# Performance work log

Measured on AMD Instinct MI355X. Metric: run time of the kernel, lower is better.

The kernel has to match this reference:

```python
import jax, jax.numpy as jnp
import numpy as np

E = 100000   # number of edges
S = 64       # multiplicity of 0e (scalar) irreps
V = 32       # multiplicity of 1o (vector) irreps; also number of gates
RS3 = 1.0 / np.sqrt(3.0)   # wigner_3j constant for (1,1,0)/(0,1,1)/(1,0,1) paths
RS6 = 1.0 / np.sqrt(6.0)   # (unused here: no 1o output from 1o x 1o)

# per-path normalization: 1/sqrt(n_paths_to_slot * mul1 * mul2), e3nn-style 'uvw'
A_SS_S = (2.0 * S * S) ** -0.5
A_VV_S = (2.0 * V * V) ** -0.5 * RS3
A_SS_G = (2.0 * S * S) ** -0.5
A_VV_G = (2.0 * V * V) ** -0.5 * RS3
A_SV_V = (2.0 * S * V) ** -0.5 * RS3
A_VS_V = (2.0 * V * S) ** -0.5 * RS3


def setup_inputs() -> dict:
    key = jax.random.key(0)
    ks = jax.random.split(key, 12)
    d_in = S + 3 * V
    return {
        "fea_in1": jax.random.normal(ks[0], (E, d_in), jnp.float32),
        "fea_in2": jax.random.normal(ks[1], (E, d_in), jnp.float32),
        "fea_weight": jax.random.normal(ks[2], (E, V), jnp.float32),   # unused (kept for signature parity)
        "batch_edge": jax.random.randint(ks[3], (E,), 0, 16, jnp.int32),  # unused (norm='')
        # SeparateWeightTensorProduct ('uvw') weights, one tensor per CG path
        "w_ss_s": jax.random.normal(ks[4], (S, S, S), jnp.float32),  # 0e x 0e -> 0e (scalars)
        "w_vv_s": jax.random.normal(ks[5], (V, V, S), jnp.float32),  # 1o x 1o -> 0e (scalars)
        "w_ss_g": jax.random.normal(ks[6], (S, S, V), jnp.float32),  # 0e x 0e -> 0e (gates)
        "w_vv_g": jax.random.normal(ks[7], (V, V, V), jnp.float32),  # 1o x 1o -> 0e (gates)
        "w_sv_v": jax.random.normal(ks[8], (S, V, V), jnp.float32),  # 0e x 1o -> 1o
        "w_vs_v": jax.random.normal(ks[9], (V, S, V), jnp.float32),  # 1o x 0e -> 1o
        # equivariant o3.Linear weights (channel mixing per irrep, shared over m)
        "wl_s": jax.random.normal(ks[10], (S, S), jnp.float32),
        "wl_v": jax.random.normal(ks[11], (V, V), jnp.float32),
    }


def reference(fea_in1, fea_in2, fea_weight, batch_edge,
              w_ss_s, w_vv_s, w_ss_g, w_vv_g, w_sv_v, w_vs_v, wl_s, wl_v):
    # split flattened irreps features: [S scalars | V vectors * 3]
    s1 = fea_in1[:, :S]
    v1 = fea_in1[:, S:].reshape(-1, V, 3)
    s2 = fea_in2[:, :S]
    v2 = fea_in2[:, S:].reshape(-1, V, 3)

    # --- separate-weight tensor product (fully connected 'uvw' paths) ---
    z_s = (A_SS_S * jnp.einsum('uvw,eu,ev->ew', w_ss_s, s1, s2)
           + A_VV_S * jnp.einsum('uvw,eui,evi->ew', w_vv_s, v1, v2))   # (E,S) 0e
    z_g = (A_SS_G * jnp.einsum('uvw,eu,ev->ew', w_ss_g, s1, s2)
           + A_VV_G * jnp.einsum('uvw,eui,evi->ew', w_vv_g, v1, v2))   # (E,V) gates 0e
    z_v = (A_SV_V * jnp.einsum('uvw,eu,evi->ewi', w_sv_v, s1, v2)
           + A_VS_V * jnp.einsum('uvw,eui,ev->ewi', w_vs_v, v1, s2))   # (E,V,3) 1o

    # --- gated nonlinearity: silu on scalars, sigmoid gates on vectors ---
    s_act = jax.nn.silu(z_s)
    v_act = jax.nn.sigmoid(z_g)[:, :, None] * z_v

    # --- equivariant linear (per-irrep channel mixing, fan-in normalized) ---
    s_out = (s_act @ wl_s) * (S ** -0.5)                    # (E,S)
    v_out = jnp.einsum('evi,vw->ewi', v_act, wl_v) * (V ** -0.5)  # (E,V,3)

    return jnp.concatenate([s_out, v_out.reshape(-1, 3 * V)], axis=-1)  # (E, S+3V)
```

## Files before the change

### kernel.cpp

```cpp
#include <hip/hip_runtime.h>


typedef _Float16 f16;
typedef _Float16 f16x8 __attribute__((ext_vector_type(8)));
typedef float    f32x4 __attribute__((ext_vector_type(4)));

constexpr float A_SS  = 0.011048543456039806f;
constexpr float A_VV  = 0.012757759747374832f;
constexpr float A_SV  = 0.009021097956087904f;
constexpr float SO_SC = 0.125f;
constexpr float VO_SC = 0.1767766952966369f;

#define MFMA16(A, B, C) __builtin_amdgcn_mfma_f32_16x16x32_f16((A), (B), (C), 0, 0, 0)

static __device__ __forceinline__ f16x8 splat8(f16 x) {
    return (f16x8){x, x, x, x, x, x, x, x};
}

__global__ void prep_weights(const float* __restrict__ wss_s, const float* __restrict__ wvv_s,
                             const float* __restrict__ wss_g, const float* __restrict__ wvv_g,
                             const float* __restrict__ wsv,   const float* __restrict__ wvs,
                             const float* __restrict__ wls,   const float* __restrict__ wlv,
                             f16* __restrict__ b1p, f16* __restrict__ b2p,
                             f16* __restrict__ wlsP, f16* __restrict__ wlvP)
{
    int idx = blockIdx.x * 256 + threadIdx.x;
    const int N1 = 160 * 6 * 512;
    const int N2 = 128 * 2 * 512;
    const int N3 = 8 * 512;
    const int N4 = 2 * 512;
    if (idx < N1) {
        int j = idx & 7, L = (idx >> 3) & 63, ct = idx >> 9;
        int t = ct % 6, c = ct / 6;
        int k = c * 32 + (L >> 4) * 8 + j;
        int n = t * 16 + (L & 15);
        float val;
        if (k < 4096) { int u = k >> 6, v = k & 63, p = u * 64 + v;
            val = A_SS * (n < 64 ? wss_s[p * 64 + n] : wss_g[p * 32 + (n - 64)]);
        } else { int k2 = k - 4096; int u = k2 >> 5, v = k2 & 31, p = u * 32 + v;
            val = A_VV * (n < 64 ? wvv_s[p * 64 + n] : wvv_g[p * 32 + (n - 64)]);
        }
        b1p[idx] = (f16)val;
    } else if (idx < N1 + N2) {
        int id2 = idx - N1;
        int j = id2 & 7, L = (id2 >> 3) & 63, ct = id2 >> 9;
        int t = ct & 1, c = ct >> 1;
        int k = c * 32 + (L >> 4) * 8 + j;
        int n = t * 16 + (L & 15);
        float val;
        if (k < 2048) { int u = k >> 5, v = k & 31; val = wsv[(u * 32 + v) * 32 + n]; }
        else { int k2 = k - 2048; int u = k2 >> 6, v = k2 & 63; val = wvs[(u * 64 + v) * 32 + n]; }
        b2p[id2] = (f16)(A_SV * val);
    } else if (idx < N1 + N2 + N3) {
        int id3 = idx - N1 - N2;
        int j = id3 & 7, L = (id3 >> 3) & 63, ct = id3 >> 9;
        int t = ct & 3, kc = ct >> 2;
        int k = kc * 32 + (L >> 4) * 8 + j;
        int n = t * 16 + (L & 15);
        wlsP[id3] = (f16)(SO_SC * wls[k * 64 + n]);
    } else if (idx < N1 + N2 + N3 + N4) {
        int id4 = idx - N1 - N2 - N3;
        int j = id4 & 7, L = (id4 >> 3) & 63, t = id4 >> 9;
        int k = (L >> 4) * 8 + j;
        int n = t * 16 + (L & 15);
        wlvP[id4] = (f16)(VO_SC * wlv[k * 32 + n]);
    }
}

__global__ __launch_bounds__(256, 3)
void seconv_mfma(const float* __restrict__ fea1, const float* __restrict__ fea2,
                 const f16* __restrict__ b1p, const f16* __restrict__ b2p,
                 const f16* __restrict__ wlsP, const f16* __restrict__ wlvP,
                 float* __restrict__ out, int E)
{
    __shared__ __align__(16) char smem[41984];
    f16*   IN   = (f16*)smem;
    f16*   zSh  = (f16*)smem;
    f16*   zGh  = (f16*)(smem + 9216);
    f16*   ZVH  = (f16*)(smem + 13568);
    float* OUTV = (float*)smem;

    const int tid  = threadIdx.x;
    const int lane = tid & 63;
    const int m    = lane & 15;
    const int quad = lane >> 4;
    const int w    = tid >> 6;
    const int h    = w & 1;
    const int nh   = w >> 1;
    const int tb   = nh * 3;
    const int e0   = blockIdx.x * 64;

    for (int i = tid; i < 64 * 160; i += 256) {
        int e = i / 160, c = i - e * 160;
        int ge = e0 + e; if (ge >= E) ge = E - 1;
        float a = fea1[ge * 160 + c];
        float b = fea2[ge * 160 + c];
        if (c < 64) { IN[e * 328 + c] = (f16)a; IN[e * 328 + 64 + c] = (f16)b; }
        else { int c2 = c - 64; int v = c2 / 3, ii = c2 - v * 3;
               IN[e * 328 + 128 + ii * 32 + v] = (f16)a;
               IN[e * 328 + 224 + ii * 32 + v] = (f16)b; }
    }
    __syncthreads();

    const int eA = h * 32 + m;
    const int eB = h * 32 + 16 + m;

    f16x8 s2q[2][2], v2q[2][3];
    #pragma unroll
    for (int p = 0; p < 2; ++p) {
        int e = p ? eB : eA;
        #pragma unroll
        for (int vh = 0; vh < 2; ++vh)
            s2q[p][vh] = *(const f16x8*)(IN + e * 328 + 64 + vh * 32 + quad * 8);
        #pragma unroll
        for (int i3 = 0; i3 < 3; ++i3)
            v2q[p][i3] = *(const f16x8*)(IN + e * 328 + 224 + i3 * 32 + quad * 8);
    }

    f32x4 acc[2][3];
    #pragma unroll
    for (int p = 0; p < 2; ++p)
        #pragma unroll
        for (int t = 0; t < 3; ++t) acc[p][t] = (f32x4){0.f, 0.f, 0.f, 0.f};

    f32x4 bcur[3], bnxt[3];
    #pragma unroll
    for (int t = 0; t < 3; ++t) bcur[t] = *(const f32x4*)(b1p + ((0 * 6 + tb + t) * 64 + lane) * 8);
    #pragma unroll
    for (int t = 0; t < 3; ++t) bnxt[t] = *(const f32x4*)(b1p + ((1 * 6 + tb + t) * 64 + lane) * 8);

    for (int ub = 0; ub < 8; ++ub) {
        f16x8 s1Ab = *(const f16x8*)(IN + eA * 328 + ub * 8);
        f16x8 s1Bb = *(const f16x8*)(IN + eB * 328 + ub * 8);
        #pragma unroll
        for (int uj = 0; uj < 8; ++uj) {
            f16x8 s1A = splat8(s1Ab[uj]);
            f16x8 s1B = splat8(s1Bb[uj]);
            #pragma unroll
            for (int vh = 0; vh < 2; ++vh) {
                int c = (ub * 8 + uj) * 2 + vh;
                f16x8 a0 = s1A * s2q[0][vh];
                f16x8 a1 = s1B * s2q[1][vh];
                f32x4 b0 = bcur[0], b1 = bcur[1], b2 = bcur[2];
                #pragma unroll
                for (int t = 0; t < 3; ++t) bcur[t] = bnxt[t];
                int cn = c + 2;
                #pragma unroll
                for (int t = 0; t < 3; ++t)
                    bnxt[t] = *(const f32x4*)(b1p + ((cn * 6 + tb + t) * 64 + lane) * 8);
                f16x8 bb0 = __builtin_bit_cast(f16x8, b0);
                f16x8 bb1 = __builtin_bit_cast(f16x8, b1);
                f16x8 bb2 = __builtin_bit_cast(f16x8, b2);
                acc[0][0] = MFMA16(a0, bb0, acc[0][0]);
                acc[0][1] = MFMA16(a0, bb1, acc[0][1]);
                acc[0][2] = MFMA16(a0, bb2, acc[0][2]);
                acc[1][0] = MFMA16(a1, bb0, acc[1][0]);
                acc[1][1] = MFMA16(a1, bb1, acc[1][1]);
                acc[1][2] = MFMA16(a1, bb2, acc[1][2]);
            }
        }
    }
    for (int ub = 0; ub < 4; ++ub) {
        f16x8 xA[3], xB[3];
        #pragma unroll
        for (int i3 = 0; i3 < 3; ++i3) {
            xA[i3] = *(const f16x8*)(IN + eA * 328 + 128 + i3 * 32 + ub * 8);
            xB[i3] = *(const f16x8*)(IN + eB * 328 + 128 + i3 * 32 + ub * 8);
        }
        #pragma unroll
        for (int uj = 0; uj < 8; ++uj) {
            int c = 128 + ub * 8 + uj;
            f16x8 a0 = splat8(xA[0][uj]) * v2q[0][0];
            a0 += splat8(xA[1][uj]) * v2q[0][1];
            a0 += splat8(xA[2][uj]) * v2q[0][2];
            f16x8 a1 = splat8(xB[0][uj]) * v2q[1][0];
            a1 += splat8(xB[1][uj]) * v2q[1][1];
            a1 += splat8(xB[2][uj]) * v2q[1][2];
            f32x4 b0 = bcur[0], b1 = bcur[1], b2 = bcur[2];
            #pragma unroll
            for (int t = 0; t < 3; ++t) bcur[t] = bnxt[t];
            int cn = c + 2; if (cn > 159) cn = 159;
            #pragma unroll
            for (int t = 0; t < 3; ++t)
                bnxt[t] = *(const f32x4*)(b1p + ((cn * 6 + tb + t) * 64 + lane) * 8);
            f16x8 bb0 = __builtin_bit_cast(f16x8, b0);
            f16x8 bb1 = __builtin_bit_cast(f16x8, b1);
            f16x8 bb2 = __builtin_bit_cast(f16x8, b2);
            acc[0][0] = MFMA16(a0, bb0, acc[0][0]);
            acc[0][1] = MFMA16(a0, bb1, acc[0][1]);
            acc[0][2] = MFMA16(a0, bb2, acc[0][2]);
            acc[1][0] = MFMA16(a1, bb0, acc[1][0]);
            acc[1][1] = MFMA16(a1, bb1, acc[1][1]);
            acc[1][2] = MFMA16(a1, bb2, acc[1][2]);
        }
    }

    const int e2 = w * 16 + m;
    f16x8 s2g[2], v2g[3];
    #pragma unroll
    for (int vh = 0; vh < 2; ++vh)
        s2g[vh] = *(const f16x8*)(IN + e2 * 328 + 64 + vh * 32 + quad * 8);
    #pragma unroll
    for (int i3 = 0; i3 < 3; ++i3)
        v2g[i3] = *(const f16x8*)(IN + e2 * 328 + 224 + i3 * 32 + quad * 8);

    f32x4 acc2[3][2];
    #pragma unroll
    for (int i3 = 0; i3 < 3; ++i3)
        #pragma unroll
        for (int t = 0; t < 2; ++t) acc2[i3][t] = (f32x4){0.f, 0.f, 0.f, 0.f};

    f32x4 q0 = *(const f32x4*)(b2p + ((0 * 2 + 0) * 64 + lane) * 8);
    f32x4 q1 = *(const f32x4*)(b2p + ((0 * 2 + 1) * 64 + lane) * 8);
    f32x4 r0 = *(const f32x4*)(b2p + ((1 * 2 + 0) * 64 + lane) * 8);
    f32x4 r1 = *(const f32x4*)(b2p + ((1 * 2 + 1) * 64 + lane) * 8);

    for (int ub = 0; ub < 8; ++ub) {
        f16x8 s1b = *(const f16x8*)(IN + e2 * 328 + ub * 8);
        #pragma unroll
        for (int uj = 0; uj < 8; ++uj) {
            int c = ub * 8 + uj;
            f16x8 bb0 = __builtin_bit_cast(f16x8, q0);
            f16x8 bb1 = __builtin_bit_cast(f16x8, q1);
            q0 = r0; q1 = r1;
            int cn = c + 2;
            r0 = *(const f32x4*)(b2p + ((cn * 2 + 0) * 64 + lane) * 8);
            r1 = *(const f32x4*)(b2p + ((cn * 2 + 1) * 64 + lane) * 8);
            f16x8 sxv = splat8(s1b[uj]);
            #pragma unroll
            for (int i3 = 0; i3 < 3; ++i3) {
                f16x8 a = sxv * v2g[i3];
                acc2[i3][0] = MFMA16(a, bb0, acc2[i3][0]);
                acc2[i3][1] = MFMA16(a, bb1, acc2[i3][1]);
            }
        }
    }
    for (int ub = 0; ub < 4; ++ub) {
        f16x8 v1b[3];
        #pragma unroll
        for (int i3 = 0; i3 < 3; ++i3)
            v1b[i3] = *(const f16x8*)(IN + e2 * 328 + 128 + i3 * 32 + ub * 8);
        #pragma unroll
        for (int uj = 0; uj < 8; ++uj) {
            f16x8 v1s0 = splat8(v1b[0][uj]);
            f16x8 v1s1 = splat8(v1b[1][uj]);
            f16x8 v1s2 = splat8(v1b[2][uj]);
            #pragma unroll
            for (int vh = 0; vh < 2; ++vh) {
                int c = 64 + (ub * 8 + uj) * 2 + vh;
                f16x8 bb0 = __builtin_bit_cast(f16x8, q0);
                f16x8 bb1 = __builtin_bit_cast(f16x8, q1);
                q0 = r0; q1 = r1;
                int cn = c + 2; if (cn > 127) cn = 127;
                r0 = *(const f32x4*)(b2p + ((cn * 2 + 0) * 64 + lane) * 8);
                r1 = *(const f32x4*)(b2p + ((cn * 2 + 1) * 64 + lane) * 8);
                f16x8 a0 = v1s0 * s2g[vh];
                f16x8 a1 = v1s1 * s2g[vh];
                f16x8 a2 = v1s2 * s2g[vh];
                acc2[0][0] = MFMA16(a0, bb0, acc2[0][0]);
                acc2[0][1] = MFMA16(a0, bb1, acc2[0][1]);
                acc2[1][0] = MFMA16(a1, bb0, acc2[1][0]);
                acc2[1][1] = MFMA16(a1, bb1, acc2[1][1]);
                acc2[2][0] = MFMA16(a2, bb0, acc2[2][0]);
                acc2[2][1] = MFMA16(a2, bb1, acc2[2][1]);
            }
        }
    }
    __syncthreads();

    #pragma unroll
    for (int p = 0; p < 2; ++p)
        #pragma unroll
        for (int t = 0; t < 3; ++t) {
            int n = (tb + t) * 16 + m;
            #pragma unroll
            for (int r = 0; r < 4; ++r) {
                int e_loc = h * 32 + p * 16 + quad * 4 + r;
                float z = acc[p][t][r];
                if (n < 64) {
                    float s = z / (1.f + __expf(-z));
                    zSh[e_loc * 72 + n] = (f16)s;
                } else {
                    zGh[e_loc * 34 + (n - 64)] = (f16)z;
                }
            }
        }
    __syncthreads();

    #pragma unroll
    for (int t = 0; t < 2; ++t)
        #pragma unroll
        for (int r = 0; r < 4; ++r) {
            int e_loc = w * 16 + quad * 4 + r;
            float zg = (float)zGh[e_loc * 34 + t * 16 + m];
            float gate = 1.f / (1.f + __expf(-zg));
            #pragma unroll
            for (int i3 = 0; i3 < 3; ++i3)
                ZVH[(i3 * 64 + e_loc) * 40 + t * 16 + m] = (f16)(gate * acc2[i3][t][r]);
        }

    {
        f32x4 accS[4];
        #pragma unroll
        for (int t = 0; t < 4; ++t) accS[t] = (f32x4){0.f, 0.f, 0.f, 0.f};
        #pragma unroll
        for (int kc = 0; kc < 2; ++kc) {
            f16x8 aS = *(const f16x8*)(zSh + (w * 16 + m) * 72 + kc * 32 + quad * 8);
            #pragma unroll
            for (int t = 0; t < 4; ++t) {
                f32x4 braw = *(const f32x4*)(wlsP + ((kc * 4 + t) * 64 + lane) * 8);
                accS[t] = MFMA16(aS, __builtin_bit_cast(f16x8, braw), accS[t]);
            }
        }
        #pragma unroll
        for (int t = 0; t < 4; ++t)
            #pragma unroll
            for (int r = 0; r < 4; ++r) {
                int ge = e0 + w * 16 + quad * 4 + r;
                if (ge < E) out[ge * 160 + t * 16 + m] = accS[t][r];
            }
    }
    {
        f32x4 accV[3][2];
        #pragma unroll
        for (int i3 = 0; i3 < 3; ++i3)
            #pragma unroll
            for (int t = 0; t < 2; ++t) accV[i3][t] = (f32x4){0.f, 0.f, 0.f, 0.f};
        f16x8 bV[2];
        #pragma unroll
        for (int t = 0; t < 2; ++t) {
            f32x4 braw = *(const f32x4*)(wlvP + (t * 64 + lane) * 8);
            bV[t] = __builtin_bit_cast(f16x8, braw);
        }
        #pragma unroll
        for (int i3 = 0; i3 < 3; ++i3) {
            f16x8 aV = *(const f16x8*)(ZVH + (i3 * 64 + w * 16 + m) * 40 + quad * 8);
            #pragma unroll
            for (int t = 0; t < 2; ++t) accV[i3][t] = MFMA16(aV, bV[t], accV[i3][t]);
        }
        __syncthreads();
        #pragma unroll
        for (int i3 = 0; i3 < 3; ++i3)
            #pragma unroll
            for (int t = 0; t < 2; ++t)
                #pragma unroll
                for (int r = 0; r < 4; ++r) {
                    int e_loc = w * 16 + quad * 4 + r;
                    OUTV[e_loc * 100 + (t * 16 + m) * 3 + i3] = accV[i3][t][r];
                }
    }
    __syncthreads();

    for (int i = tid; i < 64 * 96; i += 256) {
        int e = i / 96, c = i - e * 96;
        int ge = e0 + e;
        if (ge < E) out[ge * 160 + 64 + c] = OUTV[e * 100 + c];
    }
}

extern "C" void kernel_launch(void* const* d_in, const int* in_sizes, int n_in,
                              void* d_out, int out_size, void* d_ws, size_t ws_size,
                              hipStream_t stream) {
    const float* fea1  = (const float*)d_in[0];
    const float* fea2  = (const float*)d_in[1];
    const float* wss_s = (const float*)d_in[4];
    const float* wvv_s = (const float*)d_in[5];
    const float* wss_g = (const float*)d_in[6];
    const float* wvv_g = (const float*)d_in[7];
    const float* wsv   = (const float*)d_in[8];
    const float* wvs   = (const float*)d_in[9];
    const float* wls   = (const float*)d_in[10];
    const float* wlv   = (const float*)d_in[11];
    float* out = (float*)d_out;

    f16* b1p  = (f16*)d_ws;
    f16* b2p  = (f16*)((char*)d_ws + 983040);
    f16* wlsP = (f16*)((char*)d_ws + 1245184);
    f16* wlvP = (f16*)((char*)d_ws + 1253376);

    int E = in_sizes[0] / 160;
    int prep_total = 491520 + 131072 + 4096 + 1024;
    prep_weights<<<dim3((prep_total + 255) / 256), dim3(256), 0, stream>>>(
        wss_s, wvv_s, wss_g, wvv_g, wsv, wvs, wls, wlv, b1p, b2p, wlsP, wlvP);
    int grid = (E + 63) / 64;
    seconv_mfma<<<dim3(grid), dim3(256), 0, stream>>>(
        fea1, fea2, b1p, b2p, wlsP, wlvP, out, E);
}
```

Baseline: 427.7 us.

## Deepen weight prefetch ring, XOR-swizzle LDS staging, raise occupancy target

Replaces the two-deep register prefetch of packed B weights with a four-slot ring, so global weight loads are issued four steps ahead of their MFMA use. Moves the staged f16 input tile to a 640-byte row stride with an XOR swizzle to cut LDS bank conflicts. Shrinks shared memory and raises launch bounds to 4 blocks per SU. The deeper ring costs extra VGPRs, which works against the higher occupancy target and may cause spills.

```diff
diff --git a/kernel.cpp b/kernel.cpp
--- a/kernel.cpp
+++ b/kernel.cpp
@@ -67,14 +67,13 @@
     }
 }
 
-__global__ __launch_bounds__(256, 3)
+__global__ __launch_bounds__(256, 4)
 void seconv_mfma(const float* __restrict__ fea1, const float* __restrict__ fea2,
                  const f16* __restrict__ b1p, const f16* __restrict__ b2p,
                  const f16* __restrict__ wlsP, const f16* __restrict__ wlvP,
                  float* __restrict__ out, int E)
 {
-    __shared__ __align__(16) char smem[41984];
-    f16*   IN   = (f16*)smem;
+    __shared__ __align__(128) char smem[40960];
     f16*   zSh  = (f16*)smem;
     f16*   zGh  = (f16*)(smem + 9216);
     f16*   ZVH  = (f16*)(smem + 13568);
@@ -90,67 +89,112 @@
     const int tb   = nh * 3;
     const int e0   = blockIdx.x * 64;
 
+    auto ld8 = [&](int e, int hc) -> f16x8 {
+        int b = (e * 640 + hc * 2) ^ ((e & 7) << 4);
+        return *(const f16x8*)(smem + b);
+    };
+    auto st2 = [&](int e, int hc, f16 v) {
+        int b = (e * 640 + hc * 2) ^ ((e & 7) << 4);
+        *(f16*)(smem + b) = v;
+    };
+
     for (int i = tid; i < 64 * 160; i += 256) {
         int e = i / 160, c = i - e * 160;
         int ge = e0 + e; if (ge >= E) ge = E - 1;
         float a = fea1[ge * 160 + c];
         float b = fea2[ge * 160 + c];
-        if (c < 64) { IN[e * 328 + c] = (f16)a; IN[e * 328 + 64 + c] = (f16)b; }
+        if (c < 64) { st2(e, c, (f16)a); st2(e, 64 + c, (f16)b); }
         else { int c2 = c - 64; int v = c2 / 3, ii = c2 - v * 3;
-               IN[e * 328 + 128 + ii * 32 + v] = (f16)a;
-               IN[e * 328 + 224 + ii * 32 + v] = (f16)b; }
+               st2(e, 128 + ii * 32 + v, (f16)a);
+               st2(e, 224 + ii * 32 + v, (f16)b); }
     }
     __syncthreads();
 
     const int eA = h * 32 + m;
     const int eB = h * 32 + 16 + m;
 
-    f16x8 s2q[2][2], v2q[2][3];
-    #pragma unroll
-    for (int p = 0; p < 2; ++p) {
-        int e = p ? eB : eA;
-        #pragma unroll
-        for (int vh = 0; vh < 2; ++vh)
-            s2q[p][vh] = *(const f16x8*)(IN + e * 328 + 64 + vh * 32 + quad * 8);
-        #pragma unroll
-        for (int i3 = 0; i3 < 3; ++i3)
-            v2q[p][i3] = *(const f16x8*)(IN + e * 328 + 224 + i3 * 32 + quad * 8);
-    }
-
     f32x4 acc[2][3];
     #pragma unroll
     for (int p = 0; p < 2; ++p)
         #pragma unroll
         for (int t = 0; t < 3; ++t) acc[p][t] = (f32x4){0.f, 0.f, 0.f, 0.f};
 
-    f32x4 bcur[3], bnxt[3];
-    #pragma unroll
-    for (int t = 0; t < 3; ++t) bcur[t] = *(const f32x4*)(b1p + ((0 * 6 + tb + t) * 64 + lane) * 8);
-    #pragma unroll
-    for (int t = 0; t < 3; ++t) bnxt[t] = *(const f32x4*)(b1p + ((1 * 6 + tb + t) * 64 + lane) * 8);
-
-    for (int ub = 0; ub < 8; ++ub) {
-        f16x8 s1Ab = *(const f16x8*)(IN + eA * 328 + ub * 8);
-        f16x8 s1Bb = *(const f16x8*)(IN + eB * 328 + ub * 8);
-        #pragma unroll
-        for (int uj = 0; uj < 8; ++uj) {
-            f16x8 s1A = splat8(s1Ab[uj]);
-            f16x8 s1B = splat8(s1Bb[uj]);
-            #pragma unroll
-            for (int vh = 0; vh < 2; ++vh) {
-                int c = (ub * 8 + uj) * 2 + vh;
-                f16x8 a0 = s1A * s2q[0][vh];
-                f16x8 a1 = s1B * s2q[1][vh];
-                f32x4 b0 = bcur[0], b1 = bcur[1], b2 = bcur[2];
+    f32x4 bq[4][3];
+    #pragma unroll
+    for (int s = 0; s < 4; ++s)
+        #pragma unroll
+        for (int t = 0; t < 3; ++t)
+            bq[s][t] = *(const f32x4*)(b1p + ((s * 6 + tb + t) * 64 + lane) * 8);
+
+    {
+        f16x8 s2q[2][2];
+        #pragma unroll
+        for (int p = 0; p < 2; ++p)
+            #pragma unroll
+            for (int vh = 0; vh < 2; ++vh)
+                s2q[p][vh] = ld8(p ? eB : eA, 64 + vh * 32 + quad * 8);
+
+        for (int ub = 0; ub < 8; ++ub) {
+            f16x8 s1Ab = ld8(eA, ub * 8);
+            f16x8 s1Bb = ld8(eB, ub * 8);
+            #pragma unroll
+            for (int uj = 0; uj < 8; ++uj) {
+                f16x8 s1A = splat8(s1Ab[uj]);
+                f16x8 s1B = splat8(s1Bb[uj]);
                 #pragma unroll
-                for (int t = 0; t < 3; ++t) bcur[t] = bnxt[t];
-                int cn = c + 2;
+                for (int vh = 0; vh < 2; ++vh) {
+                    const int clo = uj * 2 + vh;
+                    const int slot = clo & 3;
+                    f16x8 bb0 = __builtin_bit_cast(f16x8, bq[slot][0]);
+                    f16x8 bb1 = __builtin_bit_cast(f16x8, bq[slot][1]);
+                    f16x8 bb2 = __builtin_bit_cast(f16x8, bq[slot][2]);
+                    int cn = ub * 16 + clo + 4;
+                    #pragma unroll
+                    for (int t = 0; t < 3; ++t)
+                        bq[slot][t] = *(const f32x4*)(b1p + ((cn * 6 + tb + t) * 64 + lane) * 8);
+                    f16x8 a0 = s1A * s2q[0][vh];
+                    f16x8 a1 = s1B * s2q[1][vh];
+                    acc[0][0] = MFMA16(a0, bb0, acc[0][0]);
+                    acc[0][1] = MFMA16(a0, bb1, acc[0][1]);
+                    acc[0][2] = MFMA16(a0, bb2, acc[0][2]);
+                    acc[1][0] = MFMA16(a1, bb0, acc[1][0]);
+                    acc[1][1] = MFMA16(a1, bb1, acc[1][1]);
+                    acc[1][2] = MFMA16(a1, bb2, acc[1][2]);
+                }
+            }
+        }
+    }
+    {
+        f16x8 v2q[2][3];
+        #pragma unroll
+        for (int p = 0; p < 2; ++p)
+            #pragma unroll
+            for (int i3 = 0; i3 < 3; ++i3)
+                v2q[p][i3] = ld8(p ? eB : eA, 224 + i3 * 32 + quad * 8);
+
+        for (int ub = 0; ub < 4; ++ub) {
+            f16x8 xA[3], xB[3];
+            #pragma unroll
+            for (int i3 = 0; i3 < 3; ++i3) {
+                xA[i3] = ld8(eA, 128 + i3 * 32 + ub * 8);
+                xB[i3] = ld8(eB, 128 + i3 * 32 + ub * 8);
+            }
+            #pragma unroll
+            for (int uj = 0; uj < 8; ++uj) {
+                const int slot = uj & 3;
+                f16x8 a0 = splat8(xA[0][uj]) * v2q[0][0];
+                a0 += splat8(xA[1][uj]) * v2q[0][1];
+                a0 += splat8(xA[2][uj]) * v2q[0][2];
+                f16x8 a1 = splat8(xB[0][uj]) * v2q[1][0];
+                a1 += splat8(xB[1][uj]) * v2q[1][1];
+                a1 += splat8(xB[2][uj]) * v2q[1][2];
+                f16x8 bb0 = __builtin_bit_cast(f16x8, bq[slot][0]);
+                f16x8 bb1 = __builtin_bit_cast(f16x8, bq[slot][1]);
+                f16x8 bb2 = __builtin_bit_cast(f16x8, bq[slot][2]);
+                int cn = 128 + ub * 8 + uj + 4; if (cn > 159) cn = 159;
                 #pragma unroll
                 for (int t = 0; t < 3; ++t)
-                    bnxt[t] = *(const f32x4*)(b1p + ((cn * 6 + tb + t) * 64 + lane) * 8);
-                f16x8 bb0 = __builtin_bit_cast(f16x8, b0);
-                f16x8 bb1 = __builtin_bit_cast(f16x8, b1);
-                f16x8 bb2 = __builtin_bit_cast(f16x8, b2);
+                    bq[slot][t] = *(const f32x4*)(b1p + ((cn * 6 + tb + t) * 64 + lane) * 8);
                 acc[0][0] = MFMA16(a0, bb0, acc[0][0]);
                 acc[0][1] = MFMA16(a0, bb1, acc[0][1]);
                 acc[0][2] = MFMA16(a0, bb2, acc[0][2]);
@@ -160,49 +204,15 @@
             }
         }
     }
-    for (int ub = 0; ub < 4; ++ub) {
-        f16x8 xA[3], xB[3];
-        #pragma unroll
-        for (int i3 = 0; i3 < 3; ++i3) {
-            xA[i3] = *(const f16x8*)(IN + eA * 328 + 128 + i3 * 32 + ub * 8);
-            xB[i3] = *(const f16x8*)(IN + eB * 328 + 128 + i3 * 32 + ub * 8);
-        }
-        #pragma unroll
-        for (int uj = 0; uj < 8; ++uj) {
-            int c = 128 + ub * 8 + uj;
-            f16x8 a0 = splat8(xA[0][uj]) * v2q[0][0];
-            a0 += splat8(xA[1][uj]) * v2q[0][1];
-            a0 += splat8(xA[2][uj]) * v2q[0][2];
-            f16x8 a1 = splat8(xB[0][uj]) * v2q[1][0];
-            a1 += splat8(xB[1][uj]) * v2q[1][1];
-            a1 += splat8(xB[2][uj]) * v2q[1][2];
-            f32x4 b0 = bcur[0], b1 = bcur[1], b2 = bcur[2];
-            #pragma unroll
-            for (int t = 0; t < 3; ++t) bcur[t] = bnxt[t];
-            int cn = c + 2; if (cn > 159) cn = 159;
-            #pragma unroll
-            for (int t = 0; t < 3; ++t)
-                bnxt[t] = *(const f32x4*)(b1p + ((cn * 6 + tb + t) * 64 + lane) * 8);
-            f16x8 bb0 = __builtin_bit_cast(f16x8, b0);
-            f16x8 bb1 = __builtin_bit_cast(f16x8, b1);
-            f16x8 bb2 = __builtin_bit_cast(f16x8, b2);
-            acc[0][0] = MFMA16(a0, bb0, acc[0][0]);
-            acc[0][1] = MFMA16(a0, bb1, acc[0][1]);
-            acc[0][2] = MFMA16(a0, bb2, acc[0][2]);
-            acc[1][0] = MFMA16(a1, bb0, acc[1][0]);
-            acc[1][1] = MFMA16(a1, bb1, acc[1][1]);
-            acc[1][2] = MFMA16(a1, bb2, acc[1][2]);
-        }
-    }
 
     const int e2 = w * 16 + m;
     f16x8 s2g[2], v2g[3];
     #pragma unroll
     for (int vh = 0; vh < 2; ++vh)
-        s2g[vh] = *(const f16x8*)(IN + e2 * 328 + 64 + vh * 32 + quad * 8);
+        s2g[vh] = ld8(e2, 64 + vh * 32 + quad * 8);
     #pragma unroll
     for (int i3 = 0; i3 < 3; ++i3)
-        v2g[i3] = *(const f16x8*)(IN + e2 * 328 + 224 + i3 * 32 + quad * 8);
+        v2g[i3] = ld8(e2, 224 + i3 * 32 + quad * 8);
 
     f32x4 acc2[3][2];
     #pragma unroll
@@ -210,22 +220,24 @@
         #pragma unroll
         for (int t = 0; t < 2; ++t) acc2[i3][t] = (f32x4){0.f, 0.f, 0.f, 0.f};
 
-    f32x4 q0 = *(const f32x4*)(b2p + ((0 * 2 + 0) * 64 + lane) * 8);
-    f32x4 q1 = *(const f32x4*)(b2p + ((0 * 2 + 1) * 64 + lane) * 8);
-    f32x4 r0 = *(const f32x4*)(b2p + ((1 * 2 + 0) * 64 + lane) * 8);
-    f32x4 r1 = *(const f32x4*)(b2p + ((1 * 2 + 1) * 64 + lane) * 8);
+    f32x4 bq2[4][2];
+    #pragma unroll
+    for (int s = 0; s < 4; ++s)
+        #pragma unroll
+        for (int t = 0; t < 2; ++t)
+            bq2[s][t] = *(const f32x4*)(b2p + ((s * 2 + t) * 64 + lane) * 8);
 
     for (int ub = 0; ub < 8; ++ub) {
-        f16x8 s1b = *(const f16x8*)(IN + e2 * 328 + ub * 8);
+        f16x8 s1b = ld8(e2, ub * 8);
         #pragma unroll
         for (int uj = 0; uj < 8; ++uj) {
-            int c = ub * 8 + uj;
-            f16x8 bb0 = __builtin_bit_cast(f16x8, q0);
-            f16x8 bb1 = __builtin_bit_cast(f16x8, q1);
-            q0 = r0; q1 = r1;
-            int cn = c + 2;
-            r0 = *(const f32x4*)(b2p + ((cn * 2 + 0) * 64 + lane) * 8);
-            r1 = *(const f32x4*)(b2p + ((cn * 2 + 1) * 64 + lane) * 8);
+            const int slot = uj & 3;
+            f16x8 bb0 = __builtin_bit_cast(f16x8, bq2[slot][0]);
+            f16x8 bb1 = __builtin_bit_cast(f16x8, bq2[slot][1]);
+            int cn = ub * 8 + uj + 4;
+            #pragma unroll
+            for (int t = 0; t < 2; ++t)
+                bq2[slot][t] = *(const f32x4*)(b2p + ((cn * 2 + t) * 64 + lane) * 8);
             f16x8 sxv = splat8(s1b[uj]);
             #pragma unroll
             for (int i3 = 0; i3 < 3; ++i3) {
@@ -239,7 +251,7 @@
         f16x8 v1b[3];
         #pragma unroll
         for (int i3 = 0; i3 < 3; ++i3)
-            v1b[i3] = *(const f16x8*)(IN + e2 * 328 + 128 + i3 * 32 + ub * 8);
+            v1b[i3] = ld8(e2, 128 + i3 * 32 + ub * 8);
         #pragma unroll
         for (int uj = 0; uj < 8; ++uj) {
             f16x8 v1s0 = splat8(v1b[0][uj]);
@@ -247,13 +259,13 @@
             f16x8 v1s2 = splat8(v1b[2][uj]);
             #pragma unroll
             for (int vh = 0; vh < 2; ++vh) {
-                int c = 64 + (ub * 8 + uj) * 2 + vh;
-                f16x8 bb0 = __builtin_bit_cast(f16x8, q0);
-                f16x8 bb1 = __builtin_bit_cast(f16x8, q1);
-                q0 = r0; q1 = r1;
-                int cn = c + 2; if (cn > 127) cn = 127;
-                r0 = *(const f32x4*)(b2p + ((cn * 2 + 0) * 64 + lane) * 8);
-                r1 = *(const f32x4*)(b2p + ((cn * 2 + 1) * 64 + lane) * 8);
+                const int slot = (uj * 2 + vh) & 3;
+                f16x8 bb0 = __builtin_bit_cast(f16x8, bq2[slot][0]);
+                f16x8 bb1 = __builtin_bit_cast(f16x8, bq2[slot][1]);
+                int cn = 64 + (ub * 8 + uj) * 2 + vh + 4; if (cn > 127) cn = 127;
+                #pragma unroll
+                for (int t = 0; t < 2; ++t)
+                    bq2[slot][t] = *(const f32x4*)(b2p + ((cn * 2 + t) * 64 + lane) * 8);
                 f16x8 a0 = v1s0 * s2g[vh];
                 f16x8 a1 = v1s1 * s2g[vh];
                 f16x8 a2 = v1s2 * s2g[vh];
```

New measurement: 455.3 us. 1.06x slower.
